# Kernel optimization log

Measured on AMD Instinct MI355X. Metric: run time of the kernel, lower is better.

## Reference

```python
import jax, jax.numpy as jnp
import numpy as np

B, T, C = 1, 2048, 2048
H, G, HS = 32, 8, 64          # heads, query groups, head size
FF = 5632                     # LLaMAMLP intermediate size
EPS = 1e-5
LEVELS = 63.0                 # 2**6 - 1 (bit=6)


@jax.custom_vjp
def _uq(x, alpha):
    xd = x / alpha
    xq = jnp.round(jnp.clip(xd, 0.0, 1.0) * LEVELS) / LEVELS
    return xq * alpha


def _uq_fwd(x, alpha):
    xd = x / alpha
    xq = jnp.round(jnp.clip(xd, 0.0, 1.0) * LEVELS) / LEVELS
    return xq * alpha, (xd, xq)


def _uq_bwd(res, g):
    xd, xq = res
    i = (xd > 1.0).astype(g.dtype)
    grad_x = g * (1.0 - i)
    grad_alpha = jnp.sum(g * (i + (xq - xd) * (1.0 - i)))
    return grad_x, grad_alpha


_uq.defvjp(_uq_fwd, _uq_bwd)


def quant_relu(x, alpha):
    return _uq(jax.nn.relu(x), alpha)


def rmsnorm(x, w):
    return w * x * jax.lax.rsqrt(jnp.mean(x * x, axis=-1, keepdims=True) + EPS)


def setup_inputs() -> dict:
    key = jax.random.key(0)
    ks = jax.random.split(key, 8)
    s = 0.02
    shape_qkv = (H + 2 * G) * HS  # 3072
    return {
        "x": jax.random.normal(ks[0], (B, T, C), jnp.float32),
        "w_rms1": jnp.ones((C,), jnp.float32),
        "w_rms2": jnp.ones((C,), jnp.float32),
        "alpha1": jnp.asarray(8.0, jnp.float32),
        "alpha2": jnp.asarray(8.0, jnp.float32),
        "alpha_q": jnp.asarray(8.0, jnp.float32),
        "alpha_sm": jnp.asarray(8.0, jnp.float32),
        "attn_w": jax.random.normal(ks[1], (shape_qkv, C), jnp.float32) * s,
        "proj_w": jax.random.normal(ks[2], (C, C), jnp.float32) * s,
        "fc1_w": jax.random.normal(ks[3], (FF, C), jnp.float32) * s,
        "fc2_w": jax.random.normal(ks[4], (FF, C), jnp.float32) * s,
        "mlp_proj_w": jax.random.normal(ks[5], (C, FF), jnp.float32) * s,
        "max_seq_length": 2048,
    }


def _attention(n1, attn_w, proj_w, alpha_q, alpha_sm):
    q_per_kv = H // G
    qkv = quant_relu(jnp.einsum('btc,oc->bto', n1, attn_w), alpha_q)
    qkv = qkv.reshape(B, T, G, q_per_kv + 2, HS)
    q = qkv[..., :q_per_kv, :].reshape(B, T, H, HS)
    k = qkv[..., q_per_kv, :]      # [B,T,G,HS]
    v = qkv[..., q_per_kv + 1, :]  # [B,T,G,HS]
    k = jnp.repeat(k, q_per_kv, axis=2)  # [B,T,H,HS]
    v = jnp.repeat(v, q_per_kv, axis=2)
    scale = 1.0 / np.sqrt(HS).astype(np.float32)
    scores = jnp.einsum('bqhd,bkhd->bhqk', q, k) * scale
    causal = jnp.tril(jnp.ones((T, T), bool))
    scores = jnp.where(causal, scores, jnp.float32(-jnp.inf))
    w = jax.nn.softmax(scores, axis=-1)
    w = quant_relu(w, alpha_sm)  # quantized softmax weights (QuantReLU on probs)
    y = jnp.einsum('bhqk,bkhd->bqhd', w, v).reshape(B, T, C)
    return jnp.einsum('btc,oc->bto', y, proj_w)


def reference(x, w_rms1, w_rms2, alpha1, alpha2, attn_w, proj_w, alpha_q,
              alpha_sm, fc1_w, fc2_w, mlp_proj_w, max_seq_length):
    n1 = quant_relu(rmsnorm(x, w_rms1), alpha1)
    h = _attention(n1, attn_w, proj_w, alpha_q, alpha_sm)
    x = x + h
    n2 = quant_relu(rmsnorm(x, w_rms2), alpha2)
    gate = jax.nn.silu(jnp.einsum('btc,fc->btf', n2, fc1_w))
    up = jnp.einsum('btc,fc->btf', n2, fc2_w)
    mlp = jnp.einsum('btf,cf->btc', gate * up, mlp_proj_w)
    return x + mlp
```

## Files before the change

### kernel.cpp

```cpp
#include <hip/hip_runtime.h>
#include <hip/hip_bf16.h>
#include <math.h>


#define T_SEQ 2048
#define C_DIM 2048
#define QKV_DIM 3072
#define FF_DIM 5632
#define FF_HALF 2816
#define LOG2E 1.44269504088896340736f

typedef short bf16x8 __attribute__((ext_vector_type(8)));
typedef float f32x4 __attribute__((ext_vector_type(4)));
typedef unsigned short u16;
typedef unsigned int u32;

__device__ __forceinline__ u16 f2bf(float f) {
  __hip_bfloat16 h = __float2bfloat16(f);
  return *reinterpret_cast<u16*>(&h);
}
__device__ __forceinline__ float bf2f(u16 u) {
  __hip_bfloat16 h;
  *reinterpret_cast<u16*>(&h) = u;
  return __bfloat162float(h);
}

__device__ __forceinline__ float qint(float v, float alpha) {
  float xd = fmaxf(v, 0.0f) / alpha;
  xd = fminf(xd, 1.0f);
  return rintf(xd * 63.0f);
}

__device__ __forceinline__ float exp2_hw(float x) {
  float r;
  asm("v_exp_f32 %0, %1" : "=v"(r) : "v"(x));
  return r;
}
__device__ __forceinline__ u32 cvtpk_bf16(float lo, float hi) {
  u32 r;
  asm("v_cvt_pk_bf16_f32 %0, %1, %2" : "=v"(r) : "v"(lo), "v"(hi));
  return r;
}

__device__ __forceinline__ void llds16(const void* g, void* l) {
  __builtin_amdgcn_global_load_lds(
      (const __attribute__((address_space(1))) unsigned int*)g,
      (__attribute__((address_space(3))) unsigned int*)l, 16, 0, 0);
}

__global__ __launch_bounds__(256) void rmsnorm_quant_int(const float* __restrict__ x,
                                                         const float* __restrict__ w,
                                                         const float* __restrict__ alpha_p,
                                                         u16* __restrict__ out) {
  const int row = blockIdx.x;
  const float* xr = x + (size_t)row * C_DIM;
  const int base = threadIdx.x * 8;
  float4 v0 = *reinterpret_cast<const float4*>(xr + base);
  float4 v1 = *reinterpret_cast<const float4*>(xr + base + 4);
  float xv[8] = {v0.x, v0.y, v0.z, v0.w, v1.x, v1.y, v1.z, v1.w};
  float ss = 0.0f;
#pragma unroll
  for (int k = 0; k < 8; ++k) ss = fmaf(xv[k], xv[k], ss);
#pragma unroll
  for (int m = 1; m < 64; m <<= 1) ss += __shfl_xor(ss, m);
  __shared__ float wsum[4];
  const int lane = threadIdx.x & 63, wv = threadIdx.x >> 6;
  if (lane == 0) wsum[wv] = ss;
  __syncthreads();
  const float tot = wsum[0] + wsum[1] + wsum[2] + wsum[3];
  const float rs = 1.0f / sqrtf(tot * (1.0f / 2048.0f) + 1e-5f);
  const float alpha = *alpha_p;
  u16 ov[8];
#pragma unroll
  for (int k = 0; k < 8; ++k) ov[k] = f2bf(qint((w[base + k] * xv[k]) * rs, alpha));
  u16* orow = out + (size_t)row * C_DIM + base;
#pragma unroll
  for (int k = 0; k < 2; ++k) {
    ushort4 u;
    u.x = ov[k * 4]; u.y = ov[k * 4 + 1]; u.z = ov[k * 4 + 2]; u.w = ov[k * 4 + 3];
    *reinterpret_cast<ushort4*>(orow + k * 4) = u;
  }
}

__global__ __launch_bounds__(256) void conv_split(const float* __restrict__ src, int ld,
                                                  int cols,
                                                  u16* __restrict__ hi, u16* __restrict__ lo) {
  const int r = blockIdx.x;
  const int c4 = (blockIdx.y * 256 + threadIdx.x) * 4;
  if (c4 >= cols) return;
  float4 v = *reinterpret_cast<const float4*>(&src[(size_t)r * ld + c4]);
  float f[4] = {v.x, v.y, v.z, v.w};
  ushort4 h, l;
  u16 hh[4], ll[4];
#pragma unroll
  for (int j = 0; j < 4; ++j) {
    hh[j] = f2bf(f[j]);
    ll[j] = f2bf(f[j] - bf2f(hh[j]));
  }
  h.x = hh[0]; h.y = hh[1]; h.z = hh[2]; h.w = hh[3];
  l.x = ll[0]; l.y = ll[1]; l.z = ll[2]; l.w = ll[3];
  const size_t o = (size_t)r * cols + c4;
  *reinterpret_cast<ushort4*>(&hi[o]) = h;
  *reinterpret_cast<ushort4*>(&lo[o]) = l;
}

template <int MODE, int EPI>
__global__ __launch_bounds__(256) void gemm_mfma(
    const u16* __restrict__ A0, const u16* __restrict__ A1,
    const u16* __restrict__ B0, const u16* __restrict__ B1,
    float* __restrict__ Cf, u16* __restrict__ Cq, const float* __restrict__ auxf,
    u16* __restrict__ p_hi, u16* __restrict__ p_lo,
    const float* __restrict__ sA_p, const float* __restrict__ aQ_p,
    int M, int N, int K) {
  constexpr int NT = (MODE == 2) ? 3 : 4;
  __shared__ __align__(16) u16 lds[2 * NT * 4096];

  const int tid = threadIdx.x;
  const int nwg = gridDim.x * gridDim.y;
  const int wg = blockIdx.y * gridDim.x + blockIdx.x;
  const int swz = (wg & 7) * (nwg >> 3) + (wg >> 3);
  const int bx = swz % gridDim.x, by = swz / gridDim.x;
  const int row0 = by * 128, col0 = bx * 128;

  const int w = tid >> 6, lane = tid & 63;
  const int wr = w >> 1, wc = w & 1;
  const int fr = lane & 15, ko = (lane >> 4) * 8;

  const int c0 = w * 128 + lane;
  const int r_a = c0 >> 2;
  const int s_a = (c0 & 3) * 8;

  u16* cu = lds;
  u16* nx = lds + NT * 4096;

  auto stage = [&](u16* base, int kt) {
    {
      const u16* g0 = A0 + (size_t)(row0 + r_a) * K + kt + s_a;
      const u16* g1 = A0 + (size_t)(row0 + r_a + 16) * K + kt + s_a;
      llds16(g0, base + (w * 128) * 8);
      llds16(g1, base + (w * 128 + 64) * 8);
    }
    if constexpr (MODE == 3) {
      const u16* g0 = A1 + (size_t)(row0 + r_a) * K + kt + s_a;
      const u16* g1 = A1 + (size_t)(row0 + r_a + 16) * K + kt + s_a;
      llds16(g0, base + 4096 + (w * 128) * 8);
      llds16(g1, base + 4096 + (w * 128 + 64) * 8);
    }
    {
      u16* dst = base + ((MODE == 2) ? 4096 : 8192);
      const u16* g0 = B0 + (size_t)(col0 + r_a) * K + kt + s_a;
      const u16* g1 = B0 + (size_t)(col0 + r_a + 16) * K + kt + s_a;
      llds16(g0, dst + (w * 128) * 8);
      llds16(g1, dst + (w * 128 + 64) * 8);
    }
    {
      u16* dst = base + ((MODE == 2) ? 8192 : 12288);
      const u16* g0 = B1 + (size_t)(col0 + r_a) * K + kt + s_a;
      const u16* g1 = B1 + (size_t)(col0 + r_a + 16) * K + kt + s_a;
      llds16(g0, dst + (w * 128) * 8);
      llds16(g1, dst + (w * 128 + 64) * 8);
    }
  };

  f32x4 acc[4][4];
  const f32x4 zero = {0.f, 0.f, 0.f, 0.f};
#pragma unroll
  for (int m = 0; m < 4; ++m)
#pragma unroll
    for (int n = 0; n < 4; ++n) acc[m][n] = zero;

  stage(cu, 0);
  __syncthreads();

  for (int kt = 0;; kt += 32) {
    const bool more = (kt + 32 < K);
    if (more) stage(nx, kt + 32);

    const u16* tA0 = cu;
    const u16* Bhi = cu + ((MODE == 2) ? 4096 : 8192);
    const u16* Blo = cu + ((MODE == 2) ? 8192 : 12288);
    bf16x8 a0f[4], bhf[4], blf[4];
#pragma unroll
    for (int m = 0; m < 4; ++m)
      a0f[m] = *reinterpret_cast<const bf16x8*>(&tA0[(wr * 64 + m * 16 + fr) * 32 + ko]);
#pragma unroll
    for (int n = 0; n < 4; ++n) {
      bhf[n] = *reinterpret_cast<const bf16x8*>(&Bhi[(wc * 64 + n * 16 + fr) * 32 + ko]);
      blf[n] = *reinterpret_cast<const bf16x8*>(&Blo[(wc * 64 + n * 16 + fr) * 32 + ko]);
    }
    if constexpr (MODE == 2) {
#pragma unroll
      for (int m = 0; m < 4; ++m)
#pragma unroll
        for (int n = 0; n < 4; ++n) {
          acc[m][n] = __builtin_amdgcn_mfma_f32_16x16x32_bf16(a0f[m], bhf[n], acc[m][n], 0, 0, 0);
          acc[m][n] = __builtin_amdgcn_mfma_f32_16x16x32_bf16(a0f[m], blf[n], acc[m][n], 0, 0, 0);
        }
    } else {
      bf16x8 a1f[4];
#pragma unroll
      for (int m = 0; m < 4; ++m)
        a1f[m] = *reinterpret_cast<const bf16x8*>(&cu[4096 + (wr * 64 + m * 16 + fr) * 32 + ko]);
#pragma unroll
      for (int m = 0; m < 4; ++m)
#pragma unroll
        for (int n = 0; n < 4; ++n) {
          acc[m][n] = __builtin_amdgcn_mfma_f32_16x16x32_bf16(a0f[m], bhf[n], acc[m][n], 0, 0, 0);
          acc[m][n] = __builtin_amdgcn_mfma_f32_16x16x32_bf16(a1f[m], bhf[n], acc[m][n], 0, 0, 0);
          acc[m][n] = __builtin_amdgcn_mfma_f32_16x16x32_bf16(a0f[m], blf[n], acc[m][n], 0, 0, 0);
        }
    }
    if (!more) break;
    __syncthreads();
    u16* t = cu; cu = nx; nx = t;
  }

  float sA = 1.0f, aQ = 1.0f;
  if constexpr (EPI == 1) { sA = (*sA_p) * (1.0f / 63.0f); aQ = *aQ_p; }
  if constexpr (EPI == 2 || EPI == 3) { sA = (*sA_p) * (1.0f / 63.0f); }
#pragma unroll
  for (int m = 0; m < 4; ++m)
#pragma unroll
    for (int n = 0; n < 4; ++n) {
      const int gcol = col0 + wc * 64 + n * 16 + fr;
#pragma unroll
      for (int j = 0; j < 4; ++j) {
        const int grow = row0 + wr * 64 + m * 16 + (lane >> 4) * 4 + j;
        const size_t idx = (size_t)grow * N + gcol;
        const float v = acc[m][n][j];
        if constexpr (EPI == 0) {
          Cf[idx] = auxf[idx] + v;
        } else if constexpr (EPI == 1) {
          float t = v * sA;
          float xd = fminf(fmaxf(t, 0.0f) / aQ, 1.0f);
          Cq[idx] = f2bf(rintf(xd * 63.0f));
        } else if constexpr (EPI == 2) {
          float t = v * sA;
          u16 h = f2bf(t);
          p_hi[idx] = h;
          p_lo[idx] = f2bf(t - bf2f(h));
        } else if constexpr (EPI == 3) {
          float gg = bf2f(p_hi[idx]) + bf2f(p_lo[idx]);
          float u = v * sA;
          float gu = (gg / (1.0f + expf(-gg))) * u;
          u16 h = f2bf(gu);
          p_hi[idx] = h;
          p_lo[idx] = f2bf(gu - bf2f(h));
        }
      }
    }
}

__global__ __launch_bounds__(256) void v_transpose(const u16* __restrict__ qkv,
                                                   u16* __restrict__ vt) {
  const int tb = blockIdx.x, g = blockIdx.y;
  const int vcol = (g * 6 + 5) * 64;
  __shared__ u16 t[64][72];
  const int tid = threadIdx.x;
#pragma unroll
  for (int i = 0; i < 2; ++i) {
    const int ch = i * 256 + tid;
    const int row = ch >> 3, c8 = (ch & 7) * 8;
    bf16x8 v = *reinterpret_cast<const bf16x8*>(
        qkv + (size_t)(tb * 64 + row) * QKV_DIM + vcol + c8);
#pragma unroll
    for (int j = 0; j < 8; ++j) t[c8 + j][row] = (u16)v[j];
  }
  __syncthreads();
#pragma unroll
  for (int i = 0; i < 2; ++i) {
    const int ch = i * 256 + tid;
    const int hs = ch >> 3, t8 = (ch & 7) * 8;
    ushort4 a, b;
    a.x = t[hs][t8];     a.y = t[hs][t8 + 1]; a.z = t[hs][t8 + 2]; a.w = t[hs][t8 + 3];
    b.x = t[hs][t8 + 4]; b.y = t[hs][t8 + 5]; b.z = t[hs][t8 + 6]; b.w = t[hs][t8 + 7];
    u16* dst = vt + (size_t)(g * 64 + hs) * T_SEQ + tb * 64 + t8;
    *reinterpret_cast<ushort4*>(dst) = a;
    *reinterpret_cast<ushort4*>(dst + 4) = b;
  }
}

__global__ __launch_bounds__(256) void attn_fused(const u16* __restrict__ qkv,
                                                  const u16* __restrict__ vt,
                                                  u16* __restrict__ y_hi,
                                                  u16* __restrict__ y_lo,
                                                  const float* __restrict__ aq_p,
                                                  const float* __restrict__ asm_p) {
  const int c = blockIdx.x;
  const int chi = c >> 8, mid = (c >> 4) & 15, clo = c & 15;
  const int h = mid + (chi << 4);
  const int qb = chi ? (15 - clo) : clo;
  const int g = h >> 2, s = h & 3;
  const int q_col = (g * 6 + s) * 64;
  const int k_col = (g * 6 + 4) * 64;

  __shared__ __align__(16) char lds_raw[49152];
  u16* Ks  = (u16*)(lds_raw + 16384);
  u16* Vts = (u16*)(lds_raw + 24576);

  const int tid = threadIdx.x;
  const int w = tid >> 6, lane = tid & 63;
  const int fr = lane & 15, gg = lane >> 4;
  char* myW = lds_raw + 32768 + w * 4096;

  const float sq = (*aq_p) * (1.0f / 63.0f);
  const float scale2 = sq * sq * 0.125f * LOG2E;
  const float alpha_sm = *asm_p;
  const float inv_a63 = 63.0f / alpha_sm;
  const float scale_y = (alpha_sm * (1.0f / 63.0f)) * sq;
  const int nkt = 2 * qb + 2;

#pragma unroll
  for (int i = 0; i < 4; ++i) {
    const int cb = (w * 4 + i) * 64;
    const int ch = cb + lane;
    const int row = ch >> 3;
    const int sb = ((ch & 7) * 16) ^ ((row & 7) << 4);
    llds16(qkv + (size_t)(qb * 128 + row) * QKV_DIM + q_col + (sb >> 1),
           lds_raw + cb * 16);
  }
  __syncthreads();
  bf16x8 qf[2][2];
#pragma unroll
  for (int nq = 0; nq < 2; ++nq)
#pragma unroll
    for (int ks = 0; ks < 2; ++ks) {
      const int qr = w * 32 + nq * 16 + fr;
      qf[nq][ks] = *reinterpret_cast<const bf16x8*>(
          lds_raw + ((qr * 128 + ks * 64 + gg * 16) ^ ((qr & 7) << 4)));
    }

  float m_run[2] = {-INFINITY, -INFINITY};
  float l_run[2] = {0.0f, 0.0f};

  for (int kt = 0; kt < nkt; ++kt) {
    __syncthreads();
#pragma unroll
    for (int i = 0; i < 2; ++i) {
      const int cb = (w * 2 + i) * 64;
      const int ch = cb + lane;
      const int row = ch >> 3;
      const int sb = ((ch & 7) * 16) ^ ((row & 7) << 4);
      llds16(qkv + (size_t)(kt * 64 + row) * QKV_DIM + k_col + (sb >> 1),
             (char*)Ks + cb * 16);
    }
    __syncthreads();
    f32x4 sac[4][2];
    const f32x4 zero = {0.f, 0.f, 0.f, 0.f};
#pragma unroll
    for (int mk = 0; mk < 4; ++mk)
#pragma unroll
      for (int nq = 0; nq < 2; ++nq) sac[mk][nq] = zero;
#pragma unroll
    for (int ks = 0; ks < 2; ++ks)
#pragma unroll
      for (int mk = 0; mk < 4; ++mk) {
        const int kr = mk * 16 + fr;
        bf16x8 kf = *reinterpret_cast<const bf16x8*>(
            (char*)Ks + ((kr * 128 + ks * 64 + gg * 16) ^ ((kr & 7) << 4)));
#pragma unroll
        for (int nq = 0; nq < 2; ++nq)
          sac[mk][nq] = __builtin_amdgcn_mfma_f32_16x16x32_bf16(kf, qf[nq][ks], sac[mk][nq], 0, 0, 0);
      }
    const bool edge = (kt >= 2 * qb);
#pragma unroll
    for (int nq = 0; nq < 2; ++nq) {
      const int qglob = qb * 128 + w * 32 + nq * 16 + fr;
      float tv[16];
#pragma unroll
      for (int mk = 0; mk < 4; ++mk)
#pragma unroll
        for (int jj = 0; jj < 4; ++jj) {
          float t = sac[mk][nq][jj] * scale2;
          if (edge && (kt * 64 + mk * 16 + gg * 4 + jj > qglob)) t = -INFINITY;
          tv[mk * 4 + jj] = t;
        }
      float vm = tv[0];
#pragma unroll
      for (int i = 1; i < 16; ++i) vm = fmaxf(vm, tv[i]);
      vm = fmaxf(vm, __shfl_xor(vm, 16));
      vm = fmaxf(vm, __shfl_xor(vm, 32));
      const float mn = fmaxf(m_run[nq], vm);
      float p = 0.0f;
#pragma unroll
      for (int i = 0; i < 16; ++i) p += exp2_hw(tv[i] - mn);
      p += __shfl_xor(p, 16);
      p += __shfl_xor(p, 32);
      l_run[nq] = l_run[nq] * exp2_hw(m_run[nq] - mn) + p;
      m_run[nq] = mn;
    }
  }

  const float linv[2] = {1.0f / l_run[0], 1.0f / l_run[1]};
  f32x4 oac[4][2];
  {
    const f32x4 zero = {0.f, 0.f, 0.f, 0.f};
#pragma unroll
    for (int mh = 0; mh < 4; ++mh)
#pragma unroll
      for (int nq = 0; nq < 2; ++nq) oac[mh][nq] = zero;
  }

  for (int kt = 0; kt < nkt; ++kt) {
    __syncthreads();
#pragma unroll
    for (int i = 0; i < 2; ++i) {
      const int cb = (w * 2 + i) * 64;
      const int ch = cb + lane;
      const int row = ch >> 3;
      const int sb = ((ch & 7) * 16) ^ ((row & 7) << 4);
      llds16(qkv + (size_t)(kt * 64 + row) * QKV_DIM + k_col + (sb >> 1),
             (char*)Ks + cb * 16);
      llds16(vt + (size_t)(g * 64 + row) * T_SEQ + kt * 64 + (sb >> 1),
             (char*)Vts + cb * 16);
    }
    __syncthreads();
    f32x4 sac[4][2];
    const f32x4 zero = {0.f, 0.f, 0.f, 0.f};
#pragma unroll
    for (int mk = 0; mk < 4; ++mk)
#pragma unroll
      for (int nq = 0; nq < 2; ++nq) sac[mk][nq] = zero;
#pragma unroll
    for (int ks = 0; ks < 2; ++ks)
#pragma unroll
      for (int mk = 0; mk < 4; ++mk) {
        const int kr = mk * 16 + fr;
        bf16x8 kf = *reinterpret_cast<const bf16x8*>(
            (char*)Ks + ((kr * 128 + ks * 64 + gg * 16) ^ ((kr & 7) << 4)));
#pragma unroll
        for (int nq = 0; nq < 2; ++nq)
          sac[mk][nq] = __builtin_amdgcn_mfma_f32_16x16x32_bf16(kf, qf[nq][ks], sac[mk][nq], 0, 0, 0);
      }
    const bool edge = (kt >= 2 * qb);
#pragma unroll
    for (int nq = 0; nq < 2; ++nq) {
      const int qglob = qb * 128 + w * 32 + nq * 16 + fr;
      const int qloc = nq * 16 + fr;
      const float mr = m_run[nq];
      const float cw = linv[nq] * inv_a63;
#pragma unroll
      for (int mk = 0; mk < 4; ++mk) {
        float lv[4];
#pragma unroll
        for (int jj = 0; jj < 4; ++jj) {
          float t = sac[mk][nq][jj] * scale2;
          if (edge && (kt * 64 + mk * 16 + gg * 4 + jj > qglob)) t = -INFINITY;
          lv[jj] = rintf(fminf(exp2_hw(t - mr) * cw, 63.0f));
        }
        const u32 pk0 = cvtpk_bf16(lv[0], lv[1]);
        const u32 pk1 = cvtpk_bf16(lv[2], lv[3]);
        const int b0 = (qloc * 128 + (mk * 16 + gg * 4) * 2) ^ ((qloc & 7) << 4);
        *reinterpret_cast<u32*>(myW + b0) = pk0;
        *reinterpret_cast<u32*>(myW + b0 + 4) = pk1;
      }
    }
#pragma unroll
    for (int ks = 0; ks < 2; ++ks) {
      bf16x8 wf[2];
#pragma unroll
      for (int nq = 0; nq < 2; ++nq) {
        const int qloc = nq * 16 + fr;
        wf[nq] = *reinterpret_cast<const bf16x8*>(
            myW + ((qloc * 128 + ks * 64 + gg * 16) ^ ((qloc & 7) << 4)));
      }
#pragma unroll
      for (int mh = 0; mh < 4; ++mh) {
        const int hr = mh * 16 + fr;
        bf16x8 vf = *reinterpret_cast<const bf16x8*>(
            (char*)Vts + ((hr * 128 + ks * 64 + gg * 16) ^ ((hr & 7) << 4)));
#pragma unroll
        for (int nq = 0; nq < 2; ++nq)
          oac[mh][nq] = __builtin_amdgcn_mfma_f32_16x16x32_bf16(vf, wf[nq], oac[mh][nq], 0, 0, 0);
      }
    }
  }

  __syncthreads();
  float* osc = (float*)(lds_raw + w * 8192);
#pragma unroll
  for (int mh = 0; mh < 4; ++mh)
#pragma unroll
    for (int nq = 0; nq < 2; ++nq) {
      const int qloc = nq * 16 + fr;
#pragma unroll
      for (int jj = 0; jj < 4; ++jj) {
        const int hs = mh * 16 + gg * 4 + jj;
        *reinterpret_cast<float*>(
            (char*)osc + ((qloc * 256 + hs * 4) ^ ((qloc & 7) << 4))) =
            oac[mh][nq][jj] * scale_y;
      }
    }
  __syncthreads();
  const int qp = lane >> 1, hf = lane & 1;
  const int qrow = qb * 128 + w * 32 + qp;
  u16* dh = y_hi + (size_t)qrow * C_DIM + h * 64 + hf * 32;
  u16* dl = y_lo + (size_t)qrow * C_DIM + h * 64 + hf * 32;
#pragma unroll
  for (int u = 0; u < 8; ++u) {
    f32x4 v = *reinterpret_cast<const f32x4*>(
        (char*)osc + ((qp * 256 + hf * 128 + u * 16) ^ ((qp & 7) << 4)));
    ushort4 hh, ll;
    u16 t0 = f2bf(v[0]); hh.x = t0; ll.x = f2bf(v[0] - bf2f(t0));
    u16 t1 = f2bf(v[1]); hh.y = t1; ll.y = f2bf(v[1] - bf2f(t1));
    u16 t2 = f2bf(v[2]); hh.z = t2; ll.z = f2bf(v[2] - bf2f(t2));
    u16 t3 = f2bf(v[3]); hh.w = t3; ll.w = f2bf(v[3] - bf2f(t3));
    *reinterpret_cast<ushort4*>(dh + u * 4) = hh;
    *reinterpret_cast<ushort4*>(dl + u * 4) = ll;
  }
}

extern "C" void kernel_launch(void* const* d_in, const int* in_sizes, int n_in,
                              void* d_out, int out_size, void* d_ws, size_t ws_size,
                              hipStream_t stream) {
  (void)in_sizes; (void)n_in; (void)out_size; (void)ws_size;
  const float* x      = (const float*)d_in[0];
  const float* w1     = (const float*)d_in[1];
  const float* w2     = (const float*)d_in[2];
  const float* a1     = (const float*)d_in[3];
  const float* a2     = (const float*)d_in[4];
  const float* aq     = (const float*)d_in[5];
  const float* a_sm   = (const float*)d_in[6];
  const float* attn_w = (const float*)d_in[7];
  const float* proj_w = (const float*)d_in[8];
  const float* fc1_w  = (const float*)d_in[9];
  const float* fc2_w  = (const float*)d_in[10];
  const float* mlp_w  = (const float*)d_in[11];
  float* out = (float*)d_out;

  char* ws = (char*)d_ws;
  u16* Whi   = (u16*)ws;
  u16* nb    = (u16*)(ws + 25165824);
  char* A    = ws + 33554432;
  u16* qkv_i = (u16*)A;
  u16* y_hi  = (u16*)(A + 12582912);
  u16* y_lo  = (u16*)(A + 20971520);
  u16* vt    = (u16*)(A + 29360128);
  u16* ghi   = (u16*)A;
  u16* glo   = (u16*)(A + 11534336);

  rmsnorm_quant_int<<<T_SEQ, 256, 0, stream>>>(x, w1, a1, nb);
  conv_split<<<dim3(QKV_DIM, 2), 256, 0, stream>>>(attn_w, C_DIM, C_DIM,
                                                   Whi, Whi + (size_t)QKV_DIM * C_DIM);
  gemm_mfma<2, 1><<<dim3(QKV_DIM / 128, T_SEQ / 128), 256, 0, stream>>>(
      nb, nullptr, Whi, Whi + (size_t)QKV_DIM * C_DIM, nullptr, qkv_i, nullptr,
      nullptr, nullptr, a1, aq, T_SEQ, QKV_DIM, C_DIM);
  v_transpose<<<dim3(32, 8), 256, 0, stream>>>(qkv_i, vt);
  attn_fused<<<512, 256, 0, stream>>>(qkv_i, vt, y_hi, y_lo, aq, a_sm);
  conv_split<<<dim3(C_DIM, 2), 256, 0, stream>>>(proj_w, C_DIM, C_DIM,
                                                 Whi, Whi + (size_t)C_DIM * C_DIM);
  gemm_mfma<3, 0><<<dim3(C_DIM / 128, T_SEQ / 128), 256, 0, stream>>>(
      y_hi, y_lo, Whi, Whi + (size_t)C_DIM * C_DIM, out, nullptr, x,
      nullptr, nullptr, nullptr, nullptr, T_SEQ, C_DIM, C_DIM);
  rmsnorm_quant_int<<<T_SEQ, 256, 0, stream>>>(out, w2, a2, nb);
  for (int h = 0; h < 2; ++h) {
    const float* fc1h = fc1_w + (size_t)h * FF_HALF * C_DIM;
    const float* fc2h = fc2_w + (size_t)h * FF_HALF * C_DIM;
    const float* mlph = mlp_w + (size_t)h * FF_HALF;
    conv_split<<<dim3(FF_HALF, 2), 256, 0, stream>>>(fc1h, C_DIM, C_DIM,
                                                     Whi, Whi + (size_t)FF_HALF * C_DIM);
    gemm_mfma<2, 2><<<dim3(FF_HALF / 128, T_SEQ / 128), 256, 0, stream>>>(
        nb, nullptr, Whi, Whi + (size_t)FF_HALF * C_DIM, nullptr, nullptr, nullptr,
        ghi, glo, a2, nullptr, T_SEQ, FF_HALF, C_DIM);
    conv_split<<<dim3(FF_HALF, 2), 256, 0, stream>>>(fc2h, C_DIM, C_DIM,
                                                     Whi, Whi + (size_t)FF_HALF * C_DIM);
    gemm_mfma<2, 3><<<dim3(FF_HALF / 128, T_SEQ / 128), 256, 0, stream>>>(
        nb, nullptr, Whi, Whi + (size_t)FF_HALF * C_DIM, nullptr, nullptr, nullptr,
        ghi, glo, a2, nullptr, T_SEQ, FF_HALF, C_DIM);
    conv_split<<<dim3(C_DIM, 3), 256, 0, stream>>>(mlph, FF_DIM, FF_HALF,
                                                   Whi, Whi + (size_t)C_DIM * FF_HALF);
    gemm_mfma<3, 0><<<dim3(C_DIM / 128, T_SEQ / 128), 256, 0, stream>>>(
        ghi, glo, Whi, Whi + (size_t)C_DIM * FF_HALF, out, nullptr, out,
        nullptr, nullptr, nullptr, nullptr, T_SEQ, C_DIM, FF_HALF);
  }
}
```

Before: 1.008 ms.

## Fuse fp32 weight hi/lo bf16 split into GEMM loads, drop conv kernels

```diff
diff --git a/kernel.cpp b/kernel.cpp
--- a/kernel.cpp
+++ b/kernel.cpp
@@ -7,11 +7,11 @@
 #define C_DIM 2048
 #define QKV_DIM 3072
 #define FF_DIM 5632
-#define FF_HALF 2816
 #define LOG2E 1.44269504088896340736f
 
 typedef short bf16x8 __attribute__((ext_vector_type(8)));
 typedef float f32x4 __attribute__((ext_vector_type(4)));
+typedef unsigned int u32x4 __attribute__((ext_vector_type(4)));
 typedef unsigned short u16;
 typedef unsigned int u32;
 
@@ -82,38 +82,17 @@
   }
 }
 
-__global__ __launch_bounds__(256) void conv_split(const float* __restrict__ src, int ld,
-                                                  int cols,
-                                                  u16* __restrict__ hi, u16* __restrict__ lo) {
-  const int r = blockIdx.x;
-  const int c4 = (blockIdx.y * 256 + threadIdx.x) * 4;
-  if (c4 >= cols) return;
-  float4 v = *reinterpret_cast<const float4*>(&src[(size_t)r * ld + c4]);
-  float f[4] = {v.x, v.y, v.z, v.w};
-  ushort4 h, l;
-  u16 hh[4], ll[4];
-#pragma unroll
-  for (int j = 0; j < 4; ++j) {
-    hh[j] = f2bf(f[j]);
-    ll[j] = f2bf(f[j] - bf2f(hh[j]));
-  }
-  h.x = hh[0]; h.y = hh[1]; h.z = hh[2]; h.w = hh[3];
-  l.x = ll[0]; l.y = ll[1]; l.z = ll[2]; l.w = ll[3];
-  const size_t o = (size_t)r * cols + c4;
-  *reinterpret_cast<ushort4*>(&hi[o]) = h;
-  *reinterpret_cast<ushort4*>(&lo[o]) = l;
-}
-
 template <int MODE, int EPI>
 __global__ __launch_bounds__(256) void gemm_mfma(
     const u16* __restrict__ A0, const u16* __restrict__ A1,
-    const u16* __restrict__ B0, const u16* __restrict__ B1,
+    const float* __restrict__ Bf,
     float* __restrict__ Cf, u16* __restrict__ Cq, const float* __restrict__ auxf,
     u16* __restrict__ p_hi, u16* __restrict__ p_lo,
     const float* __restrict__ sA_p, const float* __restrict__ aQ_p,
     int M, int N, int K) {
-  constexpr int NT = (MODE == 2) ? 3 : 4;
-  __shared__ __align__(16) u16 lds[2 * NT * 4096];
+  constexpr int BUFB = (MODE == 2) ? 24576 : 32768;
+  constexpr int BOFF = (MODE == 2) ? 8192 : 16384;
+  __shared__ __align__(16) char lds[2 * BUFB];
 
   const int tid = threadIdx.x;
   const int nwg = gridDim.x * gridDim.y;
@@ -124,41 +103,36 @@
 
   const int w = tid >> 6, lane = tid & 63;
   const int wr = w >> 1, wc = w & 1;
-  const int fr = lane & 15, ko = (lane >> 4) * 8;
+  const int fr = lane & 15, gq = lane >> 4;
 
   const int c0 = w * 128 + lane;
   const int r_a = c0 >> 2;
   const int s_a = (c0 & 3) * 8;
-
-  u16* cu = lds;
-  u16* nx = lds + NT * 4096;
-
-  auto stage = [&](u16* base, int kt) {
+  const int rB = tid >> 3;
+  const int sB0 = tid & 7;
+
+  char* cu = lds;
+  char* nx = lds + BUFB;
+
+  auto stage = [&](char* base, int kt) {
     {
       const u16* g0 = A0 + (size_t)(row0 + r_a) * K + kt + s_a;
       const u16* g1 = A0 + (size_t)(row0 + r_a + 16) * K + kt + s_a;
-      llds16(g0, base + (w * 128) * 8);
-      llds16(g1, base + (w * 128 + 64) * 8);
+      llds16(g0, base + (w * 128) * 16);
+      llds16(g1, base + (w * 128 + 64) * 16);
     }
     if constexpr (MODE == 3) {
       const u16* g0 = A1 + (size_t)(row0 + r_a) * K + kt + s_a;
       const u16* g1 = A1 + (size_t)(row0 + r_a + 16) * K + kt + s_a;
-      llds16(g0, base + 4096 + (w * 128) * 8);
-      llds16(g1, base + 4096 + (w * 128 + 64) * 8);
-    }
-    {
-      u16* dst = base + ((MODE == 2) ? 4096 : 8192);
-      const u16* g0 = B0 + (size_t)(col0 + r_a) * K + kt + s_a;
-      const u16* g1 = B0 + (size_t)(col0 + r_a + 16) * K + kt + s_a;
-      llds16(g0, dst + (w * 128) * 8);
-      llds16(g1, dst + (w * 128 + 64) * 8);
-    }
-    {
-      u16* dst = base + ((MODE == 2) ? 8192 : 12288);
-      const u16* g0 = B1 + (size_t)(col0 + r_a) * K + kt + s_a;
-      const u16* g1 = B1 + (size_t)(col0 + r_a + 16) * K + kt + s_a;
-      llds16(g0, dst + (w * 128) * 8);
-      llds16(g1, dst + (w * 128 + 64) * 8);
+      llds16(g0, base + 8192 + (w * 128) * 16);
+      llds16(g1, base + 8192 + (w * 128 + 64) * 16);
+    }
+#pragma unroll
+    for (int it = 0; it < 4; ++it) {
+      const int rowB = it * 32 + rB;
+      const int slot = sB0 ^ (rowB & 7);
+      const float* gp = Bf + (size_t)(col0 + rowB) * K + kt + slot * 4;
+      llds16(gp, base + BOFF + it * 4096 + w * 1024);
     }
   };
 
@@ -176,17 +150,35 @@
     const bool more = (kt + 32 < K);
     if (more) stage(nx, kt + 32);
 
-    const u16* tA0 = cu;
-    const u16* Bhi = cu + ((MODE == 2) ? 4096 : 8192);
-    const u16* Blo = cu + ((MODE == 2) ? 8192 : 12288);
+    const char* bufA = cu;
+    const char* bufB = cu + BOFF;
     bf16x8 a0f[4], bhf[4], blf[4];
 #pragma unroll
     for (int m = 0; m < 4; ++m)
-      a0f[m] = *reinterpret_cast<const bf16x8*>(&tA0[(wr * 64 + m * 16 + fr) * 32 + ko]);
+      a0f[m] = *reinterpret_cast<const bf16x8*>(
+          bufA + (wr * 64 + m * 16 + fr) * 64 + gq * 16);
 #pragma unroll
     for (int n = 0; n < 4; ++n) {
-      bhf[n] = *reinterpret_cast<const bf16x8*>(&Bhi[(wc * 64 + n * 16 + fr) * 32 + ko]);
-      blf[n] = *reinterpret_cast<const bf16x8*>(&Blo[(wc * 64 + n * 16 + fr) * 32 + ko]);
+      const int rowB = wc * 64 + n * 16 + fr;
+      const int bb = rowB * 128 + gq * 32;
+      const int sw = (rowB & 7) << 4;
+      f32x4 e0 = *reinterpret_cast<const f32x4*>(bufB + (bb ^ sw));
+      f32x4 e1 = *reinterpret_cast<const f32x4*>(bufB + ((bb + 16) ^ sw));
+      float e[8] = {e0[0], e0[1], e0[2], e0[3], e1[0], e1[1], e1[2], e1[3]};
+      u32 hp[4], lp[4];
+#pragma unroll
+      for (int p = 0; p < 4; ++p) {
+        const u32 u0 = __builtin_bit_cast(u32, e[2 * p]);
+        const u32 u1 = __builtin_bit_cast(u32, e[2 * p + 1]);
+        hp[p] = (u1 & 0xffff0000u) | (u0 >> 16);
+        const float l0 = e[2 * p]     - __builtin_bit_cast(float, u0 & 0xffff0000u);
+        const float l1 = e[2 * p + 1] - __builtin_bit_cast(float, u1 & 0xffff0000u);
+        lp[p] = cvtpk_bf16(l0, l1);
+      }
+      u32x4 hv = {hp[0], hp[1], hp[2], hp[3]};
+      u32x4 lv = {lp[0], lp[1], lp[2], lp[3]};
+      bhf[n] = __builtin_bit_cast(bf16x8, hv);
+      blf[n] = __builtin_bit_cast(bf16x8, lv);
     }
     if constexpr (MODE == 2) {
 #pragma unroll
@@ -200,7 +192,8 @@
       bf16x8 a1f[4];
 #pragma unroll
       for (int m = 0; m < 4; ++m)
-        a1f[m] = *reinterpret_cast<const bf16x8*>(&cu[4096 + (wr * 64 + m * 16 + fr) * 32 + ko]);
+        a1f[m] = *reinterpret_cast<const bf16x8*>(
+            cu + 8192 + (wr * 64 + m * 16 + fr) * 64 + gq * 16);
 #pragma unroll
       for (int m = 0; m < 4; ++m)
 #pragma unroll
@@ -212,7 +205,7 @@
     }
     if (!more) break;
     __syncthreads();
-    u16* t = cu; cu = nx; nx = t;
+    char* t = cu; cu = nx; nx = t;
   }
 
   float sA = 1.0f, aQ = 1.0f;
@@ -529,48 +522,32 @@
   float* out = (float*)d_out;
 
   char* ws = (char*)d_ws;
-  u16* Whi   = (u16*)ws;
-  u16* nb    = (u16*)(ws + 25165824);
-  char* A    = ws + 33554432;
-  u16* qkv_i = (u16*)A;
-  u16* y_hi  = (u16*)(A + 12582912);
-  u16* y_lo  = (u16*)(A + 20971520);
-  u16* vt    = (u16*)(A + 29360128);
-  u16* ghi   = (u16*)A;
-  u16* glo   = (u16*)(A + 11534336);
+  u16* nb    = (u16*)ws;
+  char* R    = ws + 8388608;
+  u16* qkv_i = (u16*)R;
+  u16* y_hi  = (u16*)(R + 12582912);
+  u16* y_lo  = (u16*)(R + 20971520);
+  u16* vt    = (u16*)(R + 29360128);
+  u16* ghi   = (u16*)R;
+  u16* glo   = (u16*)(R + 23068672);
 
   rmsnorm_quant_int<<<T_SEQ, 256, 0, stream>>>(x, w1, a1, nb);
-  conv_split<<<dim3(QKV_DIM, 2), 256, 0, stream>>>(attn_w, C_DIM, C_DIM,
-                                                   Whi, Whi + (size_t)QKV_DIM * C_DIM);
   gemm_mfma<2, 1><<<dim3(QKV_DIM / 128, T_SEQ / 128), 256, 0, stream>>>(
-      nb, nullptr, Whi, Whi + (size_t)QKV_DIM * C_DIM, nullptr, qkv_i, nullptr,
-      nullptr, nullptr, a1, aq, T_SEQ, QKV_DIM, C_DIM);
+      nb, nullptr, attn_w, nullptr, qkv_i, nullptr, nullptr, nullptr,
+      a1, aq, T_SEQ, QKV_DIM, C_DIM);
   v_transpose<<<dim3(32, 8), 256, 0, stream>>>(qkv_i, vt);
   attn_fused<<<512, 256, 0, stream>>>(qkv_i, vt, y_hi, y_lo, aq, a_sm);
-  conv_split<<<dim3(C_DIM, 2), 256, 0, stream>>>(proj_w, C_DIM, C_DIM,
-                                                 Whi, Whi + (size_t)C_DIM * C_DIM);
   gemm_mfma<3, 0><<<dim3(C_DIM / 128, T_SEQ / 128), 256, 0, stream>>>(
-      y_hi, y_lo, Whi, Whi + (size_t)C_DIM * C_DIM, out, nullptr, x,
-      nullptr, nullptr, nullptr, nullptr, T_SEQ, C_DIM, C_DIM);
+      y_hi, y_lo, proj_w, out, nullptr, x, nullptr, nullptr,
+      nullptr, nullptr, T_SEQ, C_DIM, C_DIM);
   rmsnorm_quant_int<<<T_SEQ, 256, 0, stream>>>(out, w2, a2, nb);
-  for (int h = 0; h < 2; ++h) {
-    const float* fc1h = fc1_w + (size_t)h * FF_HALF * C_DIM;
-    const float* fc2h = fc2_w + (size_t)h * FF_HALF * C_DIM;
-    const float* mlph = mlp_w + (size_t)h * FF_HALF;
-    conv_split<<<dim3(FF_HALF, 2), 256, 0, stream>>>(fc1h, C_DIM, C_DIM,
-                                                     Whi, Whi + (size_t)FF_HALF * C_DIM);
-    gemm_mfma<2, 2><<<dim3(FF_HALF / 128, T_SEQ / 128), 256, 0, stream>>>(
-        nb, nullptr, Whi, Whi + (size_t)FF_HALF * C_DIM, nullptr, nullptr, nullptr,
-        ghi, glo, a2, nullptr, T_SEQ, FF_HALF, C_DIM);
-    conv_split<<<dim3(FF_HALF, 2), 256, 0, stream>>>(fc2h, C_DIM, C_DIM,
-                                                     Whi, Whi + (size_t)FF_HALF * C_DIM);
-    gemm_mfma<2, 3><<<dim3(FF_HALF / 128, T_SEQ / 128), 256, 0, stream>>>(
-        nb, nullptr, Whi, Whi + (size_t)FF_HALF * C_DIM, nullptr, nullptr, nullptr,
-        ghi, glo, a2, nullptr, T_SEQ, FF_HALF, C_DIM);
-    conv_split<<<dim3(C_DIM, 3), 256, 0, stream>>>(mlph, FF_DIM, FF_HALF,
-                                                   Whi, Whi + (size_t)C_DIM * FF_HALF);
-    gemm_mfma<3, 0><<<dim3(C_DIM / 128, T_SEQ / 128), 256, 0, stream>>>(
-        ghi, glo, Whi, Whi + (size_t)C_DIM * FF_HALF, out, nullptr, out,
-        nullptr, nullptr, nullptr, nullptr, T_SEQ, C_DIM, FF_HALF);
-  }
-}
+  gemm_mfma<2, 2><<<dim3(FF_DIM / 128, T_SEQ / 128), 256, 0, stream>>>(
+      nb, nullptr, fc1_w, nullptr, nullptr, nullptr, ghi, glo,
+      a2, nullptr, T_SEQ, FF_DIM, C_DIM);
+  gemm_mfma<2, 3><<<dim3(FF_DIM / 128, T_SEQ / 128), 256, 0, stream>>>(
+      nb, nullptr, fc2_w, nullptr, nullptr, nullptr, ghi, glo,
+      a2, nullptr, T_SEQ, FF_DIM, C_DIM);
+  gemm_mfma<3, 0><<<dim3(C_DIM / 128, T_SEQ / 128), 256, 0, stream>>>(
+      ghi, glo, mlp_w, out, nullptr, out, nullptr, nullptr,
+      nullptr, nullptr, T_SEQ, C_DIM, FF_DIM);
+}
```

After: 995.8 us. About the same (-1.2%).
